# Optimization experiments

Hardware: AMD Instinct MI355X
Metric: run time of the kernel (lower is better)

## Reference

```python
import jax, jax.numpy as jnp
import numpy as np

B, T, C = 4, 2048, 1024
H = 16
D = C // H  # head_dim = 64


def setup_inputs() -> dict:
    key = jax.random.key(0)
    ks = jax.random.split(key, 9)
    s = 1.0 / np.sqrt(C)
    return {
        "x": jax.random.normal(ks[0], (B, T, C), dtype=jnp.float32),
        "wq": jax.random.uniform(ks[1], (C, C), jnp.float32, -s, s),
        "bq": jax.random.uniform(ks[2], (C,), jnp.float32, -s, s),
        "wk": jax.random.uniform(ks[3], (C, C), jnp.float32, -s, s),
        "bk": jax.random.uniform(ks[4], (C,), jnp.float32, -s, s),
        "wv": jax.random.uniform(ks[5], (C, C), jnp.float32, -s, s),
        "bv": jax.random.uniform(ks[6], (C,), jnp.float32, -s, s),
        "wo": jax.random.uniform(ks[7], (C, C), jnp.float32, -s, s),
        "bo": jax.random.uniform(ks[8], (C,), jnp.float32, -s, s),
    }


def reference(x, wq, bq, wk, bk, wv, bv, wo, bo):
    # Linear layers (torch convention: y = x @ W.T + b)
    q = x @ wq.T + bq  # [B,T,C]
    k = x @ wk.T + bk
    v = x @ wv.T + bv
    # split heads -> [B,H,T,D]
    q = q.reshape(B, T, H, D).transpose(0, 2, 1, 3)
    k = k.reshape(B, T, H, D).transpose(0, 2, 1, 3)
    v = v.reshape(B, T, H, D).transpose(0, 2, 1, 3)
    scores = jnp.einsum('bhqd,bhkd->bhqk', q, k) / jnp.sqrt(jnp.float32(D))
    causal = jnp.tril(jnp.ones((T, T), dtype=bool))  # position i attends to j<=i
    scores = jnp.where(causal, scores, -jnp.inf)
    attn = jax.nn.softmax(scores, axis=-1)
    # dropout p=0.0 (eval / identity)
    out = jnp.einsum('bhqk,bhkd->bhqd', attn, v)  # [B,H,T,D]
    out = out.transpose(0, 2, 1, 3).reshape(B, T, C)
    return out @ wo.T + bo
```

## Files before the change

### kernel.cpp

```cpp
#include <hip/hip_runtime.h>
#include <stdint.h>

#define B_DIM 4
#define T_DIM 2048
#define C_DIM 1024
#define H_DIM 16
#define D_DIM 64
#define M_DIM (B_DIM * T_DIM)
#define QK_SCALE 0.18033688011112042f

typedef float f32x4 __attribute__((ext_vector_type(4)));
typedef short bf16x8 __attribute__((ext_vector_type(8)));
typedef unsigned short u16;
typedef u16 u16x8 __attribute__((ext_vector_type(8)));

static __device__ __forceinline__ u16 f2b(float f) {
  uint32_t r;
  asm("v_cvt_pk_bf16_f32 %0, %1, %1" : "=v"(r) : "v"(f));
  return (u16)r;
}
static __device__ __forceinline__ uint32_t f2b2(float a, float b) {
  uint32_t r;
  asm("v_cvt_pk_bf16_f32 %0, %1, %2" : "=v"(r) : "v"(a), "v"(b));
  return r;
}

static __device__ __forceinline__ void gl_lds16(const u16* g, u16* l) {
  __builtin_amdgcn_global_load_lds(
      (const __attribute__((address_space(1))) void*)g,
      (__attribute__((address_space(3))) void*)l, 16, 0, 0);
}

__global__ void k_cvt(const float* __restrict__ src, u16* __restrict__ dst, int n4) {
  int i = blockIdx.x * blockDim.x + threadIdx.x;
  if (i < n4) {
    float4 v = ((const float4*)src)[i];
    uint2 o;
    o.x = f2b2(v.x, v.y);
    o.y = f2b2(v.z, v.w);
    ((uint2*)dst)[i] = o;
  }
}

__global__ void k_cvtw(const float* __restrict__ s0, const float* __restrict__ s1,
                       const float* __restrict__ s2, const float* __restrict__ s3,
                       u16* __restrict__ d0, u16* __restrict__ d1,
                       u16* __restrict__ d2, u16* __restrict__ d3) {
  int i = blockIdx.x * blockDim.x + threadIdx.x;
  int seg = i >> 18;
  int j = i & ((1 << 18) - 1);
  const float* s = seg == 0 ? s0 : seg == 1 ? s1 : seg == 2 ? s2 : s3;
  u16* d = seg == 0 ? d0 : seg == 1 ? d1 : seg == 2 ? d2 : d3;
  float4 v = ((const float4*)s)[j];
  uint2 o;
  o.x = f2b2(v.x, v.y);
  o.y = f2b2(v.z, v.w);
  ((uint2*)d)[j] = o;
}

__global__ __launch_bounds__(256) void k_gemm_qkv(
    const u16* __restrict__ A,
    const u16* __restrict__ w0, const u16* __restrict__ w1, const u16* __restrict__ w2,
    const float* __restrict__ b0, const float* __restrict__ b1, const float* __restrict__ b2,
    u16* __restrict__ Qo, u16* __restrict__ Ko, u16* __restrict__ Vo) {
  __shared__ u16 As[128 * 32];
  __shared__ u16 Bs[128 * 32];
  const int tid = threadIdx.x;
  const int l = tid & 63;
  const int w = tid >> 6;
  const int wr = w >> 1, wc = w & 1;
  const int seg = blockIdx.x >> 3;
  const int brow = blockIdx.y * 128, bcol = (blockIdx.x & 7) * 128;
  const int lrow = l & 15, lk = l >> 4;
  const int K = C_DIM;

  const u16* Bw = seg == 0 ? w0 : seg == 1 ? w1 : w2;
  const float* bias = seg == 0 ? b0 : seg == 1 ? b1 : b2;
  u16* Out = seg == 0 ? Qo : seg == 1 ? Ko : Vo;
  const float scale = seg == 0 ? QK_SCALE : 1.f;

  f32x4 acc[4][4];
  for (int m = 0; m < 4; ++m)
    for (int n = 0; n < 4; ++n)
      acc[m][n] = (f32x4){0.f, 0.f, 0.f, 0.f};

  for (int kt = 0; kt < K; kt += 32) {
    __syncthreads();
    {
      int slot = tid;
      int r0 = slot >> 2, c0 = slot & 3;
      gl_lds16(A + (size_t)(brow + r0) * K + kt + c0 * 8, As + slot * 8);
      gl_lds16(Bw + (size_t)(bcol + r0) * K + kt + c0 * 8, Bs + slot * 8);
      int slot2 = slot + 256;
      int r1 = slot2 >> 2, c1 = slot2 & 3;
      gl_lds16(A + (size_t)(brow + r1) * K + kt + c1 * 8, As + slot2 * 8);
      gl_lds16(Bw + (size_t)(bcol + r1) * K + kt + c1 * 8, Bs + slot2 * 8);
    }
    asm volatile("s_waitcnt vmcnt(0)" ::: "memory");
    __syncthreads();

    bf16x8 af[4], bfr[4];
#pragma unroll
    for (int m = 0; m < 4; ++m)
      af[m] = *(const bf16x8*)(As + (wr * 64 + m * 16 + lrow) * 32 + lk * 8);
#pragma unroll
    for (int n = 0; n < 4; ++n)
      bfr[n] = *(const bf16x8*)(Bs + (wc * 64 + n * 16 + lrow) * 32 + lk * 8);
#pragma unroll
    for (int m = 0; m < 4; ++m) {
#pragma unroll
      for (int n = 0; n < 4; ++n)
        acc[m][n] = __builtin_amdgcn_mfma_f32_16x16x32_bf16(af[m], bfr[n], acc[m][n], 0, 0, 0);
    }
  }

#pragma unroll
  for (int m = 0; m < 4; ++m) {
    int rg0 = brow + wr * 64 + m * 16 + lk * 4;
#pragma unroll
    for (int n = 0; n < 4; ++n) {
      int cg = bcol + wc * 64 + n * 16 + lrow;
      float bv = bias[cg];
#pragma unroll
      for (int i = 0; i < 4; ++i) {
        int rg = rg0 + i;
        float val = (acc[m][n][i] + bv) * scale;
        int bb = rg >> 11, tt = rg & (T_DIM - 1);
        int hh = cg >> 6, dd = cg & 63;
        Out[(((size_t)bb * H_DIM + hh) * T_DIM + tt) * D_DIM + dd] = f2b(val);
      }
    }
  }
}

__global__ __launch_bounds__(256) void k_gemm_proj(
    const u16* __restrict__ A, const u16* __restrict__ Bw,
    const float* __restrict__ bias, float* __restrict__ Cout) {
  __shared__ u16 As[128 * 32];
  __shared__ u16 Bs[128 * 32];
  const int tid = threadIdx.x;
  const int l = tid & 63;
  const int w = tid >> 6;
  const int wr = w >> 1, wc = w & 1;
  const int brow = blockIdx.y * 128, bcol = blockIdx.x * 128;
  const int lrow = l & 15, lk = l >> 4;
  const int K = C_DIM, N = C_DIM;

  f32x4 acc[4][4];
  for (int m = 0; m < 4; ++m)
    for (int n = 0; n < 4; ++n)
      acc[m][n] = (f32x4){0.f, 0.f, 0.f, 0.f};

  for (int kt = 0; kt < K; kt += 32) {
    __syncthreads();
    {
      int slot = tid;
      int r0 = slot >> 2, c0 = slot & 3;
      gl_lds16(A + (size_t)(brow + r0) * K + kt + c0 * 8, As + slot * 8);
      gl_lds16(Bw + (size_t)(bcol + r0) * K + kt + c0 * 8, Bs + slot * 8);
      int slot2 = slot + 256;
      int r1 = slot2 >> 2, c1 = slot2 & 3;
      gl_lds16(A + (size_t)(brow + r1) * K + kt + c1 * 8, As + slot2 * 8);
      gl_lds16(Bw + (size_t)(bcol + r1) * K + kt + c1 * 8, Bs + slot2 * 8);
    }
    asm volatile("s_waitcnt vmcnt(0)" ::: "memory");
    __syncthreads();

    bf16x8 af[4], bfr[4];
#pragma unroll
    for (int m = 0; m < 4; ++m)
      af[m] = *(const bf16x8*)(As + (wr * 64 + m * 16 + lrow) * 32 + lk * 8);
#pragma unroll
    for (int n = 0; n < 4; ++n)
      bfr[n] = *(const bf16x8*)(Bs + (wc * 64 + n * 16 + lrow) * 32 + lk * 8);
#pragma unroll
    for (int m = 0; m < 4; ++m) {
#pragma unroll
      for (int n = 0; n < 4; ++n)
        acc[m][n] = __builtin_amdgcn_mfma_f32_16x16x32_bf16(af[m], bfr[n], acc[m][n], 0, 0, 0);
    }
  }

#pragma unroll
  for (int m = 0; m < 4; ++m) {
    int rg0 = brow + wr * 64 + m * 16 + lk * 4;
#pragma unroll
    for (int n = 0; n < 4; ++n) {
      int cg = bcol + wc * 64 + n * 16 + lrow;
      float bv = bias[cg];
#pragma unroll
      for (int i = 0; i < 4; ++i)
        Cout[(size_t)(rg0 + i) * N + cg] = acc[m][n][i] + bv;
    }
  }
}

__global__ __launch_bounds__(256) void k_transpose(
    const u16* __restrict__ V, u16* __restrict__ Vt) {
  __shared__ u16 tile[64][65];
  const int tid = threadIdx.x;
  const int bh = blockIdx.y;
  const int t0 = blockIdx.x * 64;
  const size_t ibase = (size_t)bh * T_DIM * D_DIM + (size_t)t0 * D_DIM;
  const size_t obase = (size_t)bh * D_DIM * T_DIM + t0;

#pragma unroll
  for (int it = 0; it < 2; ++it) {
    int row = (tid >> 3) + it * 32;
    int blk = tid & 7;
    u16x8 v = *(const u16x8*)(V + ibase + (size_t)row * D_DIM + blk * 8);
#pragma unroll
    for (int j = 0; j < 8; ++j) tile[row][blk * 8 + j] = v[j];
  }
  __syncthreads();
#pragma unroll
  for (int it = 0; it < 2; ++it) {
    int d = (tid >> 3) + it * 32;
    int blk = tid & 7;
    u16x8 v;
#pragma unroll
    for (int j = 0; j < 8; ++j) v[j] = tile[blk * 8 + j][d];
    *(u16x8*)(Vt + obase + (size_t)d * T_DIM + blk * 8) = v;
  }
}

__global__ __launch_bounds__(256) void k_attn(
    const u16* __restrict__ Q, const u16* __restrict__ Kg,
    const u16* __restrict__ Vt, u16* __restrict__ O) {
  __shared__ u16 Ks[2][64 * 64];
  __shared__ u16 Vs[2][64 * 64];
  __shared__ u16 Ps[4][32 * 72];

  const int tid = threadIdx.x;
  const int l = tid & 63;
  const int w = tid >> 6;
  const int bh = blockIdx.x;
  const int qb = 15 - blockIdx.y;
  const int q0 = qb * 128;
  const int lrow = l & 15, lk = l >> 4;

  const size_t qkbase = (size_t)bh * T_DIM * D_DIM;
  const size_t vtbase = (size_t)bh * D_DIM * T_DIM;

  const int sr0 = tid >> 3, sc0 = tid & 7;
  const int sr1 = (tid + 256) >> 3, sc1 = tid & 7;
  const int kcol0 = (sc0 ^ (sr0 & 7)) * 8;
  const int kcol1 = (sc1 ^ (sr1 & 7)) * 8;

#define STAGE(buf, kt)                                                                   \
  {                                                                                      \
    gl_lds16(Kg + qkbase + (size_t)((kt) * 64 + sr0) * D_DIM + kcol0, Ks[buf] + tid * 8);\
    gl_lds16(Vt + vtbase + (size_t)sr0 * T_DIM + (kt) * 64 + kcol0, Vs[buf] + tid * 8);  \
    gl_lds16(Kg + qkbase + (size_t)((kt) * 64 + sr1) * D_DIM + kcol1,                    \
             Ks[buf] + (tid + 256) * 8);                                                 \
    gl_lds16(Vt + vtbase + (size_t)sr1 * T_DIM + (kt) * 64 + kcol1,                      \
             Vs[buf] + (tid + 256) * 8);                                                 \
  }

  bf16x8 qf[2][2];
#pragma unroll
  for (int m = 0; m < 2; ++m) {
#pragma unroll
    for (int kk = 0; kk < 2; ++kk)
      qf[m][kk] = *(const bf16x8*)(Q + qkbase +
          (size_t)(q0 + w * 32 + m * 16 + lrow) * D_DIM + kk * 32 + lk * 8);
  }

  f32x4 o[2][4];
  float m_run[2][4], l_run[2][4];
#pragma unroll
  for (int m = 0; m < 2; ++m) {
#pragma unroll
    for (int n = 0; n < 4; ++n) o[m][n] = (f32x4){0.f, 0.f, 0.f, 0.f};
#pragma unroll
    for (int i = 0; i < 4; ++i) { m_run[m][i] = -1e30f; l_run[m][i] = 0.f; }
  }

  const int diag = q0 >> 6;
  const int nkt = diag + 2;
  const int wq_hi = q0 + w * 32 + 31;

  STAGE(0, 0);

  for (int kt = 0; kt < nkt; ++kt) {
    const int cur = kt & 1;
    if (kt + 1 < nkt) {
      STAGE(cur ^ 1, kt + 1);
      asm volatile("s_waitcnt vmcnt(4)" ::: "memory");
    } else {
      asm volatile("s_waitcnt vmcnt(0)" ::: "memory");
    }
    __syncthreads();

    if (kt * 64 <= wq_hi) {
      f32x4 s[2][4];
#pragma unroll
      for (int m = 0; m < 2; ++m)
#pragma unroll
        for (int n = 0; n < 4; ++n) s[m][n] = (f32x4){0.f, 0.f, 0.f, 0.f};

#pragma unroll
      for (int kk = 0; kk < 2; ++kk) {
        bf16x8 kf[4];
#pragma unroll
        for (int n = 0; n < 4; ++n) {
          int row = n * 16 + lrow;
          int blk = (kk * 4 + lk) ^ (row & 7);
          kf[n] = *(const bf16x8*)(Ks[cur] + row * 64 + blk * 8);
        }
#pragma unroll
        for (int m = 0; m < 2; ++m) {
#pragma unroll
          for (int n = 0; n < 4; ++n)
            s[m][n] = __builtin_amdgcn_mfma_f32_16x16x32_bf16(qf[m][kk], kf[n], s[m][n], 0, 0, 0);
        }
      }

      if (kt >= diag) {
#pragma unroll
        for (int m = 0; m < 2; ++m) {
#pragma unroll
          for (int i = 0; i < 4; ++i) {
            int qg = q0 + w * 32 + m * 16 + lk * 4 + i;
#pragma unroll
            for (int n = 0; n < 4; ++n) {
              int kg = kt * 64 + n * 16 + lrow;
              if (kg > qg) s[m][n][i] = -1e30f;
            }
          }
        }
      }

#pragma unroll
      for (int m = 0; m < 2; ++m) {
        float pm[4], rs[4];
#pragma unroll
        for (int i = 0; i < 4; ++i)
          pm[i] = fmaxf(fmaxf(s[m][0][i], s[m][1][i]), fmaxf(s[m][2][i], s[m][3][i]));
#pragma unroll
        for (int off = 1; off < 16; off <<= 1) {
#pragma unroll
          for (int i = 0; i < 4; ++i)
            pm[i] = fmaxf(pm[i], __shfl_xor(pm[i], off, 64));
        }
        bool grow = false;
#pragma unroll
        for (int i = 0; i < 4; ++i) grow = grow || (pm[i] > m_run[m][i] + 8.f);
        if (__any(grow)) {
#pragma unroll
          for (int i = 0; i < 4; ++i) {
            float mn = fmaxf(m_run[m][i], pm[i]);
            float sc = exp2f(m_run[m][i] - mn);
            m_run[m][i] = mn;
            l_run[m][i] *= sc;
#pragma unroll
            for (int n = 0; n < 4; ++n) o[m][n][i] *= sc;
          }
        }
#pragma unroll
        for (int i = 0; i < 4; ++i) rs[i] = 0.f;
#pragma unroll
        for (int n = 0; n < 4; ++n) {
#pragma unroll
          for (int i = 0; i < 4; ++i) {
            float p = exp2f(s[m][n][i] - m_run[m][i]);
            s[m][n][i] = p;
            rs[i] += p;
          }
        }
#pragma unroll
        for (int off = 1; off < 16; off <<= 1) {
#pragma unroll
          for (int i = 0; i < 4; ++i)
            rs[i] += __shfl_xor(rs[i], off, 64);
        }
#pragma unroll
        for (int i = 0; i < 4; ++i) l_run[m][i] += rs[i];

#pragma unroll
        for (int n = 0; n < 4; ++n) {
#pragma unroll
          for (int i = 0; i < 4; ++i) {
            int prow = m * 16 + lk * 4 + i;
            Ps[w][prow * 72 + n * 16 + lrow] = f2b(s[m][n][i]);
          }
        }
      }

#pragma unroll
      for (int kk = 0; kk < 2; ++kk) {
        bf16x8 pf[2], vf[4];
#pragma unroll
        for (int m = 0; m < 2; ++m)
          pf[m] = *(const bf16x8*)(&Ps[w][(m * 16 + lrow) * 72 + kk * 32 + lk * 8]);
#pragma unroll
        for (int n = 0; n < 4; ++n) {
          int row = n * 16 + lrow;
          int blk = (kk * 4 + lk) ^ (row & 7);
          vf[n] = *(const bf16x8*)(Vs[cur] + row * 64 + blk * 8);
        }
#pragma unroll
        for (int m = 0; m < 2; ++m) {
#pragma unroll
          for (int n = 0; n < 4; ++n)
            o[m][n] = __builtin_amdgcn_mfma_f32_16x16x32_bf16(pf[m], vf[n], o[m][n], 0, 0, 0);
        }
      }
    }
    __syncthreads();
  }

  const int bb = bh >> 4, hh = bh & 15;
#pragma unroll
  for (int m = 0; m < 2; ++m) {
#pragma unroll
    for (int i = 0; i < 4; ++i) {
      int t = q0 + w * 32 + m * 16 + lk * 4 + i;
      float inv = 1.f / l_run[m][i];
#pragma unroll
      for (int n = 0; n < 4; ++n) {
        O[((size_t)bb * T_DIM + t) * C_DIM + hh * D_DIM + n * 16 + lrow] =
            f2b(o[m][n][i] * inv);
      }
    }
  }
}

extern "C" void kernel_launch(void* const* d_in, const int* in_sizes, int n_in,
                              void* d_out, int out_size, void* d_ws, size_t ws_size,
                              hipStream_t stream) {
  (void)in_sizes; (void)n_in; (void)out_size; (void)ws_size;
  const float* x  = (const float*)d_in[0];
  const float* wq = (const float*)d_in[1];
  const float* bq = (const float*)d_in[2];
  const float* wk = (const float*)d_in[3];
  const float* bk = (const float*)d_in[4];
  const float* wv = (const float*)d_in[5];
  const float* bv = (const float*)d_in[6];
  const float* wo = (const float*)d_in[7];
  const float* bo = (const float*)d_in[8];
  float* out = (float*)d_out;

  u16* xb  = (u16*)d_ws;
  u16* wqb = xb + (size_t)M_DIM * C_DIM;
  u16* wkb = wqb + (size_t)C_DIM * C_DIM;
  u16* wvb = wkb + (size_t)C_DIM * C_DIM;
  u16* wob = wvb + (size_t)C_DIM * C_DIM;
  u16* Qb  = wob + (size_t)C_DIM * C_DIM;
  u16* Kb  = Qb + (size_t)M_DIM * C_DIM;
  u16* Vb  = Kb + (size_t)M_DIM * C_DIM;
  u16* Vtb = Vb + (size_t)M_DIM * C_DIM;
  u16* Ob  = Vb;

  int n4x = M_DIM * C_DIM / 4;
  k_cvt<<<(n4x + 255) / 256, 256, 0, stream>>>(x, xb, n4x);
  k_cvtw<<<4096, 256, 0, stream>>>(wq, wk, wv, wo, wqb, wkb, wvb, wob);

  k_gemm_qkv<<<dim3(24, M_DIM / 128), 256, 0, stream>>>(
      xb, wqb, wkb, wvb, bq, bk, bv, Qb, Kb, Vb);

  k_transpose<<<dim3(T_DIM / 64, B_DIM * H_DIM), 256, 0, stream>>>(Vb, Vtb);
  k_attn<<<dim3(B_DIM * H_DIM, 16), 256, 0, stream>>>(Qb, Kb, Vtb, Ob);
  k_gemm_proj<<<dim3(C_DIM / 128, M_DIM / 128), 256, 0, stream>>>(Ob, wob, bo, out);
}
```

Measured before the change: 242.5 us.

## Rewrite attention with transposed 32x32x16 MFMA, keeping P in registers

The attention kernel now computes S^T = K·Q^T with 32x32x16 bf16 MFMAs, so each lane owns one query row. The row max and row sum then need only a single cross-half shuffle instead of four-step butterflies. P is converted to bf16 and rearranged into the B-operand layout with lane-xor-32 shuffles rather than going through an LDS staging buffer, and the output is accumulated as O^T = V^T·P^T. This removes the Ps shared memory, its writes and reads, and most shuffle reductions, at the cost of more register pressure from the 16-wide accumulators and a different causal-mask indexing.

```diff
diff --git a/kernel.cpp b/kernel.cpp
--- a/kernel.cpp
+++ b/kernel.cpp
@@ -10,6 +10,7 @@
 #define QK_SCALE 0.18033688011112042f
 
 typedef float f32x4 __attribute__((ext_vector_type(4)));
+typedef float f32x16 __attribute__((ext_vector_type(16)));
 typedef short bf16x8 __attribute__((ext_vector_type(8)));
 typedef unsigned short u16;
 typedef u16 u16x8 __attribute__((ext_vector_type(8)));
@@ -229,7 +230,6 @@
     const u16* __restrict__ Vt, u16* __restrict__ O) {
   __shared__ u16 Ks[2][64 * 64];
   __shared__ u16 Vs[2][64 * 64];
-  __shared__ u16 Ps[4][32 * 72];
 
   const int tid = threadIdx.x;
   const int l = tid & 63;
@@ -237,15 +237,18 @@
   const int bh = blockIdx.x;
   const int qb = 15 - blockIdx.y;
   const int q0 = qb * 128;
-  const int lrow = l & 15, lk = l >> 4;
+  const int ql = l & 31;
+  const int hi = l >> 5;
+  const int r0 = q0 + w * 32;
+  const int qg = r0 + ql;
 
   const size_t qkbase = (size_t)bh * T_DIM * D_DIM;
   const size_t vtbase = (size_t)bh * D_DIM * T_DIM;
 
-  const int sr0 = tid >> 3, sc0 = tid & 7;
-  const int sr1 = (tid + 256) >> 3, sc1 = tid & 7;
-  const int kcol0 = (sc0 ^ (sr0 & 7)) * 8;
-  const int kcol1 = (sc1 ^ (sr1 & 7)) * 8;
+  const int sr0 = tid >> 3, sc = tid & 7;
+  const int sr1 = (tid + 256) >> 3;
+  const int kcol0 = (sc ^ (sr0 & 7)) * 8;
+  const int kcol1 = (sc ^ (sr1 & 7)) * 8;
 
 #define STAGE(buf, kt)                                                                   \
   {                                                                                      \
@@ -257,28 +260,20 @@
              Vs[buf] + (tid + 256) * 8);                                                 \
   }
 
-  bf16x8 qf[2][2];
-#pragma unroll
-  for (int m = 0; m < 2; ++m) {
-#pragma unroll
-    for (int kk = 0; kk < 2; ++kk)
-      qf[m][kk] = *(const bf16x8*)(Q + qkbase +
-          (size_t)(q0 + w * 32 + m * 16 + lrow) * D_DIM + kk * 32 + lk * 8);
-  }
-
-  f32x4 o[2][4];
-  float m_run[2][4], l_run[2][4];
-#pragma unroll
-  for (int m = 0; m < 2; ++m) {
-#pragma unroll
-    for (int n = 0; n < 4; ++n) o[m][n] = (f32x4){0.f, 0.f, 0.f, 0.f};
-#pragma unroll
-    for (int i = 0; i < 4; ++i) { m_run[m][i] = -1e30f; l_run[m][i] = 0.f; }
-  }
-
-  const int diag = q0 >> 6;
-  const int nkt = diag + 2;
-  const int wq_hi = q0 + w * 32 + 31;
+  bf16x8 qf[4];
+#pragma unroll
+  for (int kk = 0; kk < 4; ++kk)
+    qf[kk] = *(const bf16x8*)(Q + qkbase + (size_t)qg * D_DIM + kk * 16 + hi * 8);
+
+  f32x16 oacc[2];
+#pragma unroll
+  for (int dt = 0; dt < 2; ++dt)
+#pragma unroll
+    for (int r = 0; r < 16; ++r) oacc[dt][r] = 0.f;
+  float m_run = -1e30f, l_run = 0.f;
+
+  const int tdiag = r0 >> 6;
+  const int nkt = (q0 >> 6) + 2;
 
   STAGE(0, 0);
 
@@ -292,136 +287,110 @@
     }
     __syncthreads();
 
-    if (kt * 64 <= wq_hi) {
-      f32x4 s[2][4];
-#pragma unroll
-      for (int m = 0; m < 2; ++m)
-#pragma unroll
-        for (int n = 0; n < 4; ++n) s[m][n] = (f32x4){0.f, 0.f, 0.f, 0.f};
-
-#pragma unroll
-      for (int kk = 0; kk < 2; ++kk) {
-        bf16x8 kf[4];
-#pragma unroll
-        for (int n = 0; n < 4; ++n) {
-          int row = n * 16 + lrow;
-          int blk = (kk * 4 + lk) ^ (row & 7);
-          kf[n] = *(const bf16x8*)(Ks[cur] + row * 64 + blk * 8);
+    if (kt <= tdiag) {
+      f32x16 s[2];
+#pragma unroll
+      for (int a = 0; a < 2; ++a)
+#pragma unroll
+        for (int r = 0; r < 16; ++r) s[a][r] = 0.f;
+
+#pragma unroll
+      for (int kk = 0; kk < 4; ++kk) {
+#pragma unroll
+        for (int a = 0; a < 2; ++a) {
+          int row = a * 32 + ql;
+          int blk = (kk * 2 + hi) ^ (row & 7);
+          bf16x8 kf = *(const bf16x8*)(Ks[cur] + row * 64 + blk * 8);
+          s[a] = __builtin_amdgcn_mfma_f32_32x32x16_bf16(kf, qf[kk], s[a], 0, 0, 0);
         }
-#pragma unroll
-        for (int m = 0; m < 2; ++m) {
-#pragma unroll
-          for (int n = 0; n < 4; ++n)
-            s[m][n] = __builtin_amdgcn_mfma_f32_16x16x32_bf16(qf[m][kk], kf[n], s[m][n], 0, 0, 0);
-        }
-      }
-
-      if (kt >= diag) {
-#pragma unroll
-        for (int m = 0; m < 2; ++m) {
-#pragma unroll
-          for (int i = 0; i < 4; ++i) {
-            int qg = q0 + w * 32 + m * 16 + lk * 4 + i;
-#pragma unroll
-            for (int n = 0; n < 4; ++n) {
-              int kg = kt * 64 + n * 16 + lrow;
-              if (kg > qg) s[m][n][i] = -1e30f;
-            }
+      }
+
+      if (kt == tdiag) {
+#pragma unroll
+        for (int a = 0; a < 2; ++a) {
+#pragma unroll
+          for (int r = 0; r < 16; ++r) {
+            int kv = kt * 64 + a * 32 + (r & 3) + 8 * (r >> 2) + 4 * hi;
+            if (kv > qg) s[a][r] = -1e30f;
           }
         }
       }
 
-#pragma unroll
-      for (int m = 0; m < 2; ++m) {
-        float pm[4], rs[4];
-#pragma unroll
-        for (int i = 0; i < 4; ++i)
-          pm[i] = fmaxf(fmaxf(s[m][0][i], s[m][1][i]), fmaxf(s[m][2][i], s[m][3][i]));
-#pragma unroll
-        for (int off = 1; off < 16; off <<= 1) {
-#pragma unroll
-          for (int i = 0; i < 4; ++i)
-            pm[i] = fmaxf(pm[i], __shfl_xor(pm[i], off, 64));
+      float t[16];
+#pragma unroll
+      for (int r = 0; r < 16; ++r) t[r] = fmaxf(s[0][r], s[1][r]);
+#pragma unroll
+      for (int r = 0; r < 8; ++r) t[r] = fmaxf(t[r], t[r + 8]);
+#pragma unroll
+      for (int r = 0; r < 4; ++r) t[r] = fmaxf(t[r], t[r + 4]);
+      float pm = fmaxf(fmaxf(t[0], t[1]), fmaxf(t[2], t[3]));
+      pm = fmaxf(pm, __shfl_xor(pm, 32, 64));
+
+      if (__any(pm > m_run + 8.f)) {
+        float mn = fmaxf(m_run, pm);
+        float sc = exp2f(m_run - mn);
+        m_run = mn;
+        l_run *= sc;
+#pragma unroll
+        for (int dt = 0; dt < 2; ++dt)
+#pragma unroll
+          for (int r = 0; r < 16; ++r) oacc[dt][r] *= sc;
+      }
+
+      float rs0 = 0.f, rs1 = 0.f, rs2 = 0.f, rs3 = 0.f;
+#pragma unroll
+      for (int a = 0; a < 2; ++a) {
+#pragma unroll
+        for (int r = 0; r < 16; ++r) {
+          float p = exp2f(s[a][r] - m_run);
+          s[a][r] = p;
+          if ((r & 3) == 0) rs0 += p;
+          else if ((r & 3) == 1) rs1 += p;
+          else if ((r & 3) == 2) rs2 += p;
+          else rs3 += p;
         }
-        bool grow = false;
-#pragma unroll
-        for (int i = 0; i < 4; ++i) grow = grow || (pm[i] > m_run[m][i] + 8.f);
-        if (__any(grow)) {
-#pragma unroll
-          for (int i = 0; i < 4; ++i) {
-            float mn = fmaxf(m_run[m][i], pm[i]);
-            float sc = exp2f(m_run[m][i] - mn);
-            m_run[m][i] = mn;
-            l_run[m][i] *= sc;
-#pragma unroll
-            for (int n = 0; n < 4; ++n) o[m][n][i] *= sc;
-          }
+      }
+      float rs = (rs0 + rs1) + (rs2 + rs3);
+      rs += __shfl_xor(rs, 32, 64);
+      l_run += rs;
+
+#pragma unroll
+      for (int kk = 0; kk < 4; ++kk) {
+        const int a = kk >> 1;
+        const int base = (kk & 1) * 8;
+        union { uint32_t wd[4]; bf16x8 v; } pf;
+#pragma unroll
+        for (int i = 0; i < 2; ++i) {
+          uint32_t Aw = f2b2(s[a][base + 2 * i], s[a][base + 2 * i + 1]);
+          uint32_t Bw = f2b2(s[a][base + 4 + 2 * i], s[a][base + 5 + 2 * i]);
+          uint32_t As_ = (uint32_t)__shfl_xor((int)Aw, 32, 64);
+          uint32_t Bs_ = (uint32_t)__shfl_xor((int)Bw, 32, 64);
+          pf.wd[i] = hi ? Bs_ : Aw;
+          pf.wd[2 + i] = hi ? Bw : As_;
         }
 #pragma unroll
-        for (int i = 0; i < 4; ++i) rs[i] = 0.f;
-#pragma unroll
-        for (int n = 0; n < 4; ++n) {
-#pragma unroll
-          for (int i = 0; i < 4; ++i) {
-            float p = exp2f(s[m][n][i] - m_run[m][i]);
-            s[m][n][i] = p;
-            rs[i] += p;
-          }
+        for (int dt = 0; dt < 2; ++dt) {
+          int row = dt * 32 + ql;
+          int blk = (kk * 2 + hi) ^ (row & 7);
+          bf16x8 vf = *(const bf16x8*)(Vs[cur] + row * 64 + blk * 8);
+          oacc[dt] = __builtin_amdgcn_mfma_f32_32x32x16_bf16(vf, pf.v, oacc[dt], 0, 0, 0);
         }
-#pragma unroll
-        for (int off = 1; off < 16; off <<= 1) {
-#pragma unroll
-          for (int i = 0; i < 4; ++i)
-            rs[i] += __shfl_xor(rs[i], off, 64);
-        }
-#pragma unroll
-        for (int i = 0; i < 4; ++i) l_run[m][i] += rs[i];
-
-#pragma unroll
-        for (int n = 0; n < 4; ++n) {
-#pragma unroll
-          for (int i = 0; i < 4; ++i) {
-            int prow = m * 16 + lk * 4 + i;
-            Ps[w][prow * 72 + n * 16 + lrow] = f2b(s[m][n][i]);
-          }
-        }
-      }
-
-#pragma unroll
-      for (int kk = 0; kk < 2; ++kk) {
-        bf16x8 pf[2], vf[4];
-#pragma unroll
-        for (int m = 0; m < 2; ++m)
-          pf[m] = *(const bf16x8*)(&Ps[w][(m * 16 + lrow) * 72 + kk * 32 + lk * 8]);
-#pragma unroll
-        for (int n = 0; n < 4; ++n) {
-          int row = n * 16 + lrow;
-          int blk = (kk * 4 + lk) ^ (row & 7);
-          vf[n] = *(const bf16x8*)(Vs[cur] + row * 64 + blk * 8);
-        }
-#pragma unroll
-        for (int m = 0; m < 2; ++m) {
-#pragma unroll
-          for (int n = 0; n < 4; ++n)
-            o[m][n] = __builtin_amdgcn_mfma_f32_16x16x32_bf16(pf[m], vf[n], o[m][n], 0, 0, 0);
-        }
       }
     }
     __syncthreads();
   }
 
   const int bb = bh >> 4, hh = bh & 15;
-#pragma unroll
-  for (int m = 0; m < 2; ++m) {
-#pragma unroll
-    for (int i = 0; i < 4; ++i) {
-      int t = q0 + w * 32 + m * 16 + lk * 4 + i;
-      float inv = 1.f / l_run[m][i];
-#pragma unroll
-      for (int n = 0; n < 4; ++n) {
-        O[((size_t)bb * T_DIM + t) * C_DIM + hh * D_DIM + n * 16 + lrow] =
-            f2b(o[m][n][i] * inv);
-      }
+  const float inv = 1.f / l_run;
+  u16* orow = O + ((size_t)bb * T_DIM + qg) * C_DIM + hh * D_DIM;
+#pragma unroll
+  for (int dt = 0; dt < 2; ++dt) {
+#pragma unroll
+    for (int g = 0; g < 4; ++g) {
+      uint2 val;
+      val.x = f2b2(oacc[dt][g * 4 + 0] * inv, oacc[dt][g * 4 + 1] * inv);
+      val.y = f2b2(oacc[dt][g * 4 + 2] * inv, oacc[dt][g * 4 + 3] * inv);
+      *(uint2*)(orow + dt * 32 + g * 8 + 4 * hi) = val;
     }
   }
 }
```

After: 202.7 us. 16.4% less time.
